# Kernel optimization log

Measured on AMD Instinct MI355X. Metric: run time of the kernel, lower is better.

## Reference

```python
import jax, jax.numpy as jnp
import numpy as np

N_HASHES = 8
BUCKET_SIZE = 64


def setup_inputs() -> dict:
    key = jax.random.key(0)
    k1, k2, k3 = jax.random.split(key, 3)
    B, S, D = 16, 4096, 64
    n_buckets = S // BUCKET_SIZE  # 64
    qk = jax.random.normal(k1, (B, S, D), jnp.float32)
    v = jax.random.normal(k2, (B, S, D), jnp.float32)
    # random rotations (shared across batch, per hash round): (1, D, n_hashes, n_buckets//2)
    rotations = jax.random.normal(k3, (1, D, N_HASHES, n_buckets // 2), jnp.float32)
    return {"qk": qk, "v": v, "rotations": rotations}


def _look_one_back(x):
    # concat each chunk with the previous chunk (wrap-around), along the within-chunk axis
    x_extra = jnp.roll(x, 1, axis=1)
    return jnp.concatenate([x, x_extra], axis=2)


def _lsh_attention(qk, v, rotations):
    B, S, D = qk.shape
    n_buckets = S // BUCKET_SIZE

    # ---- hash_vectors ----
    rot = jnp.broadcast_to(rotations, (B, D, N_HASHES, n_buckets // 2))
    rotated = jnp.einsum('btf,bfhi->bhti', qk, rot)           # [B, H, S, nb/2]
    rotated = jnp.concatenate([rotated, -rotated], axis=-1)    # [B, H, S, nb]
    buckets = jnp.argmax(rotated, axis=-1)                     # [B, H, S]
    offsets = (jnp.arange(N_HASHES) * n_buckets).reshape(1, -1, 1)
    buckets = (buckets + offsets).reshape(B, -1)               # [B, H*S]

    # ---- sort by (bucket, position) ----
    total = N_HASHES * S
    ticker = jnp.arange(total)
    buckets_and_t = S * buckets + (ticker % S)[None, :]        # unique keys
    sticker = jnp.argsort(buckets_and_t, axis=-1)              # sort order
    undo_sort = jnp.argsort(sticker, axis=-1)

    st = sticker % S                                           # original positions
    sqk = jnp.take_along_axis(qk, st[..., None], axis=1)       # [B, H*S, D]
    sv = jnp.take_along_axis(v, st[..., None], axis=1)

    chunk_size = N_HASHES * n_buckets                          # number of chunks
    bq_t = st.reshape(B, chunk_size, -1)                       # [B, C, bs]
    bqk = sqk.reshape(B, chunk_size, -1, D)                    # [B, C, bs, D]
    bv = sv.reshape(B, chunk_size, -1, D)

    bq = bqk
    bk = bqk / jnp.clip(jnp.linalg.norm(bqk, axis=-1, keepdims=True), 1e-12)

    bk = _look_one_back(bk)                                    # [B, C, 2*bs, D]
    bv = _look_one_back(bv)
    bkv_t = _look_one_back(bq_t)                               # [B, C, 2*bs]

    dots = jnp.einsum('bhie,bhje->bhij', bq, bk) * (D ** -0.5)  # [B, C, bs, 2*bs]

    # mask self-attention (token attending to itself)
    self_mask = bq_t[:, :, :, None] == bkv_t[:, :, None, :]
    dots = jnp.where(self_mask, jnp.float32(-1e5), dots)

    lse = jax.nn.logsumexp(dots, axis=-1, keepdims=True)
    probs = jnp.exp(dots - lse)
    bo = jnp.einsum('buij,buje->buie', probs, bv)              # [B, C, bs, D]

    so = bo.reshape(B, -1, D)                                  # [B, H*S, D]
    slogits = lse.reshape(B, -1)                               # [B, H*S]

    # unsort back to original order
    o = jnp.take_along_axis(so, undo_sort[..., None], axis=1)
    logits = jnp.take_along_axis(slogits, undo_sort, axis=1)

    o = o.reshape(B, N_HASHES, S, D)
    logits = logits.reshape(B, N_HASHES, S, 1)

    # combine hash rounds by normalized logsumexp weights
    w = jnp.exp(logits - jax.nn.logsumexp(logits, axis=1, keepdims=True))
    out = jnp.sum(o * w, axis=1)                               # [B, S, D]
    return out, buckets


def reference(qk, v, rotations):
    return _lsh_attention(qk, v, rotations)
```

## Files before the change

kernel.cpp:

```cpp
#include <hip/hip_runtime.h>
#include <hip/hip_bf16.h>
#include <math.h>

#define B 16
#define S 4096
#define D 64
#define NH 8
#define NBUCK 64
#define CHUNKS 512
#define BS 64

#define GAP_MFMA 0.12f

typedef __attribute__((ext_vector_type(8))) short s8_t;
typedef __attribute__((ext_vector_type(4))) float f4_t;
typedef __attribute__((ext_vector_type(2))) unsigned int u32x2;

__device__ inline unsigned short bf16_rne(float x) {
    unsigned int u = __float_as_uint(x);
    u += 0x7fffu + ((u >> 16) & 1u);
    return (unsigned short)(u >> 16);
}
__device__ inline unsigned int pack_bf16_pair(float x0, float x1) {
    return (unsigned int)bf16_rne(x0) | ((unsigned int)bf16_rne(x1) << 16);
}
__device__ inline void split_bf16(float x, unsigned short& h, unsigned short& l) {
    h = bf16_rne(x);
    float hf = __uint_as_float(((unsigned int)h) << 16);
    l = bf16_rne(x - hf);
}
__device__ inline unsigned int pack_trunc(float x0, float x1) {
    return __builtin_amdgcn_perm(__float_as_uint(x1), __float_as_uint(x0),
                                 0x07060302u);
}
__device__ inline unsigned short bf16_trunc(float x) {
    return (unsigned short)(__float_as_uint(x) >> 16);
}

#define BAR_LGKM() do {                                          \
    asm volatile("s_waitcnt lgkmcnt(0)" ::: "memory");           \
    __builtin_amdgcn_s_barrier();                                \
    asm volatile("" ::: "memory");                               \
} while (0)

template<int OFF>
__device__ inline u32x2 tr_read(unsigned int vaddr) {
    u32x2 d;
    asm volatile("ds_read_b64_tr_b16 %0, %1 offset:%c2"
                 : "=v"(d) : "v"(vaddr), "i"(OFF));
    return d;
}

#define HA_OFF 0
#define HQH_OFF 36864
#define HQL_OFF 55296
#define HLDS_TOT 73728
#define HSTR 144

__global__ __launch_bounds__(256, 2) void hash_kernel(
    const float* __restrict__ qk, const float* __restrict__ rot,
    float* __restrict__ out_buckets, int* __restrict__ bucket_ws,
    unsigned char* __restrict__ flag_ws)
{
    __shared__ char lds[HLDS_TOT];
    int tid = threadIdx.x;
    int wg = blockIdx.x;
    int orig = ((wg & 7) << 6) + (wg >> 3);
    int b    = orig >> 5;
    int tile = orig & 31;
    int token0 = tile * 128;

    {
        char* arow = lds + HA_OFF + tid * HSTR;
        #pragma unroll 4
        for (int f = 0; f < 64; f += 2) {
            float r0 = rot[(size_t)f * 256 + tid];
            float r1 = rot[(size_t)(f + 1) * 256 + tid];
            *(unsigned int*)(arow + f * 2) = pack_bf16_pair(r0, r1);
        }
    }
    {
        int wv0   = tid >> 6;
        int lane0 = tid & 63;
        int s_ = lane0 & 3;
        int rowA = wv0 * 32 + (lane0 >> 2);
        int rowB = rowA + 16;
        const float4* qA = (const float4*)(qk + ((size_t)b * S + token0 + rowA) * D);
        const float4* qB = (const float4*)(qk + ((size_t)b * S + token0 + rowB) * D);
        float4 a4[4], b4[4];
        #pragma unroll
        for (int n = 0; n < 4; ++n) { a4[n] = qA[n * 4 + s_]; b4[n] = qB[n * 4 + s_]; }

        char* qhA = lds + HQH_OFF + rowA * HSTR;
        char* qlA = lds + HQL_OFF + rowA * HSTR;
        char* qhB = lds + HQH_OFF + rowB * HSTR;
        char* qlB = lds + HQL_OFF + rowB * HSTR;
        #pragma unroll
        for (int n = 0; n < 4; ++n) {
            float fa[4] = {a4[n].x, a4[n].y, a4[n].z, a4[n].w};
            float fb[4] = {b4[n].x, b4[n].y, b4[n].z, b4[n].w};
            unsigned short h[4], l[4];
            #pragma unroll
            for (int e = 0; e < 4; ++e) split_bf16(fa[e], h[e], l[e]);
            *(uint2*)(qhA + n * 32 + s_ * 8) =
                make_uint2((unsigned)h[0] | ((unsigned)h[1] << 16),
                           (unsigned)h[2] | ((unsigned)h[3] << 16));
            *(uint2*)(qlA + n * 32 + s_ * 8) =
                make_uint2((unsigned)l[0] | ((unsigned)l[1] << 16),
                           (unsigned)l[2] | ((unsigned)l[3] << 16));
            #pragma unroll
            for (int e = 0; e < 4; ++e) split_bf16(fb[e], h[e], l[e]);
            *(uint2*)(qhB + n * 32 + s_ * 8) =
                make_uint2((unsigned)h[0] | ((unsigned)h[1] << 16),
                           (unsigned)h[2] | ((unsigned)h[3] << 16));
            *(uint2*)(qlB + n * 32 + s_ * 8) =
                make_uint2((unsigned)l[0] | ((unsigned)l[1] << 16),
                           (unsigned)l[2] | ((unsigned)l[3] << 16));
        }
    }
    __syncthreads();

    int wv   = tid >> 6;
    int lane = tid & 63;
    int quad = lane >> 4;
    int cc   = lane & 15;

    for (int nt = 0; nt < 2; ++nt) {
        int ntg = wv * 2 + nt;
        const char* qrh = lds + HQH_OFF + (ntg * 16 + cc) * HSTR + quad * 16;
        const char* qrl = lds + HQL_OFF + (ntg * 16 + cc) * HSTR + quad * 16;
        s8_t bh0 = *(const s8_t*)(qrh);
        s8_t bh1 = *(const s8_t*)(qrh + 64);
        s8_t bl0 = *(const s8_t*)(qrl);
        s8_t bl1 = *(const s8_t*)(qrl + 64);

        float v1 = -3e38f, v2 = -3e38f;
        int i1 = 0;

        for (int mt = 0; mt < 16; ++mt) {
            const char* arow = lds + HA_OFF + (mt * 16 + cc) * HSTR + quad * 16;
            s8_t a0 = *(const s8_t*)(arow);
            s8_t a1 = *(const s8_t*)(arow + 64);
            f4_t acc = (f4_t){0.f, 0.f, 0.f, 0.f};
            acc = __builtin_amdgcn_mfma_f32_16x16x32_bf16(a0, bh0, acc, 0, 0, 0);
            acc = __builtin_amdgcn_mfma_f32_16x16x32_bf16(a1, bh1, acc, 0, 0, 0);
            acc = __builtin_amdgcn_mfma_f32_16x16x32_bf16(a0, bl0, acc, 0, 0, 0);
            acc = __builtin_amdgcn_mfma_f32_16x16x32_bf16(a1, bl1, acc, 0, 0, 0);

            if ((mt & 1) == 0) { v1 = -3e38f; v2 = -3e38f; i1 = 0; }
            int ibase = ((mt & 1) << 4) + (quad << 2);
            #pragma unroll
            for (int r = 0; r < 4; ++r) {
                float vp = acc[r];
                int ip = ibase + r;
                v2 = fmaxf(v2, fminf(vp, v1));
                if (vp > v1) { v1 = vp; i1 = ip; }
                float vn = -vp;
                v2 = fmaxf(v2, fminf(vn, v1));
                if (vn > v1) { v1 = vn; i1 = ip + 32; }
            }

            if (mt & 1) {
                #pragma unroll
                for (int off = 16; off <= 32; off <<= 1) {
                    float ov1 = __shfl_xor(v1, off, 64);
                    float ov2 = __shfl_xor(v2, off, 64);
                    int   oi1 = __shfl_xor(i1, off, 64);
                    float nv2 = fmaxf(fmaxf(v2, ov2), fminf(v1, ov1));
                    if (ov1 > v1) { v1 = ov1; i1 = oi1; }
                    v2 = nv2;
                }
                if (quad == 0) {
                    int h = mt >> 1;
                    int tok = token0 + ntg * 16 + cc;
                    size_t idx = (size_t)(b * NH + h) * S + tok;
                    bucket_ws[idx] = i1;
                    out_buckets[idx] = (float)(i1 + h * NBUCK);
                    flag_ws[idx] = (v1 - v2 < GAP_MFMA) ? 1 : 0;
                }
            }
        }
    }
}

__global__ __launch_bounds__(256) void hash_fixup_kernel(
    const float* __restrict__ qk, const float* __restrict__ rot,
    const unsigned char* __restrict__ flag_ws,
    float* __restrict__ out_buckets, int* __restrict__ bucket_ws)
{
    __shared__ int list[2048];
    __shared__ int cnt;
    int tid = threadIdx.x;
    if (tid == 0) cnt = 0;
    __syncthreads();

    int base = blockIdx.x * 2048;
    for (int i = tid; i < 2048; i += 256) {
        if (flag_ws[base + i]) {
            int slot = atomicAdd(&cnt, 1);
            list[slot] = base + i;
        }
    }
    __syncthreads();
    int n = cnt;

    for (int j = tid; j < n; j += 256) {
        int gid = list[j];
        int bh = gid >> 12, t = gid & (S - 1);
        int b = bh >> 3, h = bh & 7;
        const float* row = qk + ((size_t)b * S + t) * D;

        double acc[32];
        #pragma unroll
        for (int i = 0; i < 32; ++i) acc[i] = 0.0;
        for (int f = 0; f < 64; ++f) {
            double x = (double)row[f];
            const float* rr = rot + f * (NH * 32) + h * 32;
            #pragma unroll
            for (int i = 0; i < 32; ++i)
                acc[i] = __fma_rn(x, (double)rr[i], acc[i]);
        }
        double best = acc[0]; int bi = 0;
        double worst = acc[0]; int wi = 0;
        #pragma unroll
        for (int i = 1; i < 32; ++i) {
            if (acc[i] > best)  { best = acc[i]; bi = i; }
            if (acc[i] < worst) { worst = acc[i]; wi = i; }
        }
        int bucket = (-worst > best) ? (32 + wi) : bi;
        bucket_ws[gid] = bucket;
        out_buckets[gid] = (float)(bucket + h * NBUCK);
    }
}

__global__ __launch_bounds__(512) void sort_kernel(
    const int* __restrict__ bucket_ws, int* __restrict__ st_ws)
{
    __shared__ int sb[S];
    __shared__ int hist[8][64];
    __shared__ int bpref[64];
    __shared__ int woff[8][64];

    int tid  = threadIdx.x;
    int wv   = tid >> 6;
    int lane = tid & 63;
    int base = blockIdx.x * S;

    hist[wv][lane] = 0;
    __syncthreads();

    int qbase = wv * 512;
    #pragma unroll
    for (int i = 0; i < 8; ++i) {
        int t = qbase + i * 64 + lane;
        int v = bucket_ws[base + t];
        sb[t] = v;
        atomicAdd(&hist[wv][v], 1);
    }
    __syncthreads();

    if (wv == 0) {
        int total = 0;
        #pragma unroll
        for (int w = 0; w < 8; ++w) total += hist[w][lane];
        int x = total;
        #pragma unroll
        for (int off = 1; off < 64; off <<= 1) {
            int y = __shfl_up(x, off, 64);
            if (lane >= off) x += y;
        }
        bpref[lane] = x - total;
    }
    __syncthreads();
    {
        int o = bpref[lane];
        for (int w2 = 0; w2 < 8; ++w2) {
            if (w2 < wv) o += hist[w2][lane];
        }
        woff[wv][lane] = o;
    }
    __syncthreads();

    for (int g = 0; g < 8; ++g) {
        int t = qbase + g * 64 + lane;
        int v = sb[t];

        unsigned long long m = ~0ULL;
        #pragma unroll
        for (int bit = 0; bit < 6; ++bit) {
            unsigned long long bm = __ballot((v >> bit) & 1);
            m &= ((v >> bit) & 1) ? bm : ~bm;
        }
        unsigned long long below = (lane == 63) ? ~0ULL >> 1
                                 : ((1ULL << lane) - 1ULL);
        int rank = __popcll(m & below);
        int cnt  = __popcll(m);

        int pos = woff[wv][v] + rank;
        st_ws[base + pos] = t;

        if ((m & below) == 0ULL)
            woff[wv][v] += cnt;
    }
}

#define OFF_VT 18432
#define OFF_NRM 35840
#define OFF_TKX 36352
#define OFF_PINV 36864
#define LDS_TOT 37120
#define KSTRB 144
#define PSTRB 272

template<int KC>
__device__ inline void pv_step(const char* lds, unsigned vaddr,
                               int wv, int cc, int quad, f4_t* oaccT)
{
    s8_t pb = *(const s8_t*)(lds + (wv * 16 + cc) * PSTRB + KC * 64 + quad * 16);
    u32x2 t00 = tr_read<KC * 4352 +    0>(vaddr);
    u32x2 t01 = tr_read<KC * 4352 +  544>(vaddr);
    u32x2 t10 = tr_read<KC * 4352 + 1088>(vaddr);
    u32x2 t11 = tr_read<KC * 4352 + 1632>(vaddr);
    u32x2 t20 = tr_read<KC * 4352 + 2176>(vaddr);
    u32x2 t21 = tr_read<KC * 4352 + 2720>(vaddr);
    u32x2 t30 = tr_read<KC * 4352 + 3264>(vaddr);
    u32x2 t31 = tr_read<KC * 4352 + 3808>(vaddr);
    asm volatile("s_waitcnt lgkmcnt(0)" ::: "memory");
    __builtin_amdgcn_sched_barrier(0);
    union { u32x2 d[2]; s8_t s; } u0, u1, u2, u3;
    u0.d[0] = t00; u0.d[1] = t01;
    u1.d[0] = t10; u1.d[1] = t11;
    u2.d[0] = t20; u2.d[1] = t21;
    u3.d[0] = t30; u3.d[1] = t31;
    oaccT[0] = __builtin_amdgcn_mfma_f32_16x16x32_bf16(u0.s, pb, oaccT[0], 0, 0, 0);
    oaccT[1] = __builtin_amdgcn_mfma_f32_16x16x32_bf16(u1.s, pb, oaccT[1], 0, 0, 0);
    oaccT[2] = __builtin_amdgcn_mfma_f32_16x16x32_bf16(u2.s, pb, oaccT[2], 0, 0, 0);
    oaccT[3] = __builtin_amdgcn_mfma_f32_16x16x32_bf16(u3.s, pb, oaccT[3], 0, 0, 0);
}

__global__ __launch_bounds__(256, 4) void attn_kernel(
    const float* __restrict__ qk, const float* __restrict__ v,
    const int* __restrict__ st_ws,
    __hip_bfloat16* __restrict__ o_ws, float* __restrict__ logits_ws)
{
    __shared__ char lds[LDS_TOT];
    float* nrm_s  = (float*)(lds + OFF_NRM);
    int*   tkx    = (int*)(lds + OFF_TKX);
    float* pinv_s = (float*)(lds + OFF_PINV);

    int tid = threadIdx.x;
    int wg = blockIdx.x;
    int orig = ((wg & 7) << 10) + (wg >> 3);
    int c = orig & (CHUNKS - 1);
    int b = orig >> 9;
    int h = c >> 6;
    int sbase = b * (NH * S);
    int cprev = (c + CHUNKS - 1) & (CHUNKS - 1);

    int wv   = tid >> 6;
    int lane = tid & 63;
    int quad = lane >> 4;
    int cc   = lane & 15;
    int s_   = lane & 3;

    int rowA = wv * 32 + (lane >> 2);
    int rowB = rowA + 16;
    int chK  = (wv < 2) ? c : cprev;
    int tokKA = st_ws[sbase + chK * BS + (rowA & 63)];
    int tokKB = st_ws[sbase + chK * BS + (rowB & 63)];
    const float4* kpA = (const float4*)(qk + ((size_t)b * S + tokKA) * D);
    const float4* kpB = (const float4*)(qk + ((size_t)b * S + tokKB) * D);
    float4 kA4[4], kB4[4];
    #pragma unroll
    for (int n = 0; n < 4; ++n) { kA4[n] = kpA[n * 4 + s_]; kB4[n] = kpB[n * 4 + s_]; }

    int prA = wv * 32 + (lane >> 2);
    int prB = prA + 16;
    int ciA = ((prA & 3) << 4) | (prA >> 3);
    int ciB = ((prB & 3) << 4) | (prB >> 3);
    int chVA = (prA & 4) ? cprev : c;
    int chVB = (prB & 4) ? cprev : c;
    int tokVA = st_ws[sbase + chVA * BS + ciA];
    int tokVB = st_ws[sbase + chVB * BS + ciB];
    const float4* vpA = (const float4*)(v + ((size_t)b * S + tokVA) * D);
    const float4* vpB = (const float4*)(v + ((size_t)b * S + tokVB) * D);
    float4 vA4[4], vB4[4];
    #pragma unroll
    for (int n = 0; n < 4; ++n) { vA4[n] = vpA[n * 4 + s_]; vB4[n] = vpB[n * 4 + s_]; }

    {
        float ssA = 0.f, ssB = 0.f;
        #pragma unroll
        for (int n = 0; n < 4; ++n) {
            ssA += kA4[n].x*kA4[n].x + kA4[n].y*kA4[n].y
                 + kA4[n].z*kA4[n].z + kA4[n].w*kA4[n].w;
            ssB += kB4[n].x*kB4[n].x + kB4[n].y*kB4[n].y
                 + kB4[n].z*kB4[n].z + kB4[n].w*kB4[n].w;
        }
        ssA += __shfl_xor(ssA, 1, 64); ssA += __shfl_xor(ssA, 2, 64);
        ssB += __shfl_xor(ssB, 1, 64); ssB += __shfl_xor(ssB, 2, 64);
        if (s_ == 0) {
            nrm_s[rowA] = __builtin_amdgcn_rsqf(fmaxf(ssA, 1e-24f)) * 0.18033688f;
            nrm_s[rowB] = __builtin_amdgcn_rsqf(fmaxf(ssB, 1e-24f)) * 0.18033688f;
            tkx[rowA] = tokKA;
            tkx[rowB] = tokKB;
        }
        #pragma unroll
        for (int n = 0; n < 4; ++n) {
            *(uint2*)(lds + rowA * KSTRB + n * 32 + s_ * 8) =
                make_uint2(pack_trunc(kA4[n].x, kA4[n].y),
                           pack_trunc(kA4[n].z, kA4[n].w));
            *(uint2*)(lds + rowB * KSTRB + n * 32 + s_ * 8) =
                make_uint2(pack_trunc(kB4[n].x, kB4[n].y),
                           pack_trunc(kB4[n].z, kB4[n].w));
        }
    }
    BAR_LGKM();

    int qrow = wv * 16 + cc;
    f4_t acc[8];
    #pragma unroll
    for (int t = 0; t < 8; ++t) acc[t] = (f4_t){0.f,0.f,0.f,0.f};

    __builtin_amdgcn_s_setprio(1);
    #pragma unroll
    for (int kc = 0; kc < 2; ++kc) {
        int aoff = kc * 64 + quad * 16;
        s8_t av = *(const s8_t*)(lds + qrow * KSTRB + aoff);
        #pragma unroll
        for (int t = 0; t < 8; ++t) {
            s8_t bv = *(const s8_t*)(lds + (t * 16 + cc) * KSTRB + aoff);
            acc[t] = __builtin_amdgcn_mfma_f32_16x16x32_bf16(av, bv, acc[t], 0, 0, 0);
        }
    }
    __builtin_amdgcn_s_setprio(0);

    {
        int kcA = prA >> 5, qA = (prA >> 3) & 3, rA = (prA >> 2) & 1, jA = prA & 3;
        int kcB = prB >> 5, qB = (prB >> 3) & 3, rB = (prB >> 2) & 1, jB = prB & 3;
        #pragma unroll
        for (int n = 0; n < 4; ++n) {
            *(uint2*)(lds + OFF_VT + (kcA * 8 + n * 2 + rA) * 544
                      + qA * 128 + jA * 32 + s_ * 8) =
                make_uint2(pack_trunc(vA4[n].x, vA4[n].y),
                           pack_trunc(vA4[n].z, vA4[n].w));
            *(uint2*)(lds + OFF_VT + (kcB * 8 + n * 2 + rB) * 544
                      + qB * 128 + jB * 32 + s_ * 8) =
                make_uint2(pack_trunc(vB4[n].x, vB4[n].y),
                           pack_trunc(vB4[n].z, vB4[n].w));
        }
    }

    float invsc[8];
    #pragma unroll
    for (int t = 0; t < 8; ++t)
        invsc[t] = nrm_s[t * 16 + cc];

    float sm[4] = {0.f, 0.f, 0.f, 0.f};
    #pragma unroll
    for (int t = 0; t < 8; ++t) {
        #pragma unroll
        for (int g = 0; g < 4; ++g)
            acc[t][g] = __builtin_amdgcn_exp2f(acc[t][g] * invsc[t]);
        if (t == wv) {
            #pragma unroll
            for (int g = 0; g < 4; ++g)
                if (cc == quad * 4 + g) acc[t][g] = 0.f;
        }
        #pragma unroll
        for (int g = 0; g < 4; ++g) sm[g] += acc[t][g];
    }
    #pragma unroll
    for (int msk = 1; msk <= 8; msk <<= 1)
        #pragma unroll
        for (int g = 0; g < 4; ++g) sm[g] += __shfl_xor(sm[g], msk, 64);

    if (cc == 0) {
        #pragma unroll
        for (int g = 0; g < 4; ++g) {
            int q = wv * 16 + quad * 4 + g;
            int tq = tkx[q];
            pinv_s[q] = __builtin_amdgcn_rcpf(sm[g]);
            logits_ws[sbase + h * S + tq] = 0.69314718f * __log2f(sm[g]);
        }
    }

    BAR_LGKM();
    #pragma unroll
    for (int g = 0; g < 4; ++g) {
        int q = wv * 16 + quad * 4 + g;
        uint4 w;
        w.x = pack_trunc(acc[0][g], acc[1][g]);
        w.y = pack_trunc(acc[2][g], acc[3][g]);
        w.z = pack_trunc(acc[4][g], acc[5][g]);
        w.w = pack_trunc(acc[6][g], acc[7][g]);
        *(uint4*)(lds + q * PSTRB + cc * 16) = w;
    }

    f4_t oaccT[4];
    #pragma unroll
    for (int n = 0; n < 4; ++n) oaccT[n] = (f4_t){0.f,0.f,0.f,0.f};

    unsigned vaddr = (unsigned)(unsigned long long)(lds + OFF_VT)
                   + (unsigned)lane * 8u;

    __builtin_amdgcn_s_setprio(1);
    pv_step<0>(lds, vaddr, wv, cc, quad, oaccT);
    pv_step<1>(lds, vaddr, wv, cc, quad, oaccT);
    pv_step<2>(lds, vaddr, wv, cc, quad, oaccT);
    pv_step<3>(lds, vaddr, wv, cc, quad, oaccT);
    __builtin_amdgcn_s_setprio(0);

    {
        int q = wv * 16 + cc;
        int tok = tkx[q];
        float pq = pinv_s[q];
        __hip_bfloat16* op = o_ws + ((size_t)(sbase + h * S + tok)) * D + quad * 4;
        #pragma unroll
        for (int n = 0; n < 4; ++n) {
            uint2 pk2;
            pk2.x = pack_trunc(oaccT[n][0] * pq, oaccT[n][1] * pq);
            pk2.y = pack_trunc(oaccT[n][2] * pq, oaccT[n][3] * pq);
            *(uint2*)(op + n * 16) = pk2;
        }
    }
}

__global__ __launch_bounds__(256) void combine_kernel(
    const __hip_bfloat16* __restrict__ o_ws, const float* __restrict__ logits_ws,
    float* __restrict__ out)
{
    int gid = blockIdx.x * 256 + threadIdx.x;
    int token = gid >> 3;
    int d8 = gid & 7;
    int b = token >> 12;
    int t = token & (S - 1);
    int base = b * (NH * S) + t;

    float l[8];
    #pragma unroll
    for (int hh = 0; hh < 8; ++hh) l[hh] = logits_ws[base + hh * S];
    float m = l[0];
    #pragma unroll
    for (int hh = 1; hh < 8; ++hh) m = fmaxf(m, l[hh]);
    float w[8]; float ssum = 0.f;
    #pragma unroll
    for (int hh = 0; hh < 8; ++hh) { w[hh] = __expf(l[hh] - m); ssum += w[hh]; }
    float inv = __builtin_amdgcn_rcpf(ssum);

    float accv[8] = {0,0,0,0,0,0,0,0};
    #pragma unroll
    for (int hh = 0; hh < 8; ++hh) {
        uint4 pk = *(const uint4*)(o_ws + (size_t)(base + hh * S) * D + d8 * 8);
        float wh = w[hh] * inv;
        unsigned int ws_[4] = {pk.x, pk.y, pk.z, pk.w};
        #pragma unroll
        for (int e = 0; e < 4; ++e) {
            float lo = __uint_as_float(ws_[e] << 16);
            float hi = __uint_as_float(ws_[e] & 0xffff0000u);
            accv[2*e]   += wh * lo;
            accv[2*e+1] += wh * hi;
        }
    }
    float4* op = (float4*)(out + (size_t)token * D + d8 * 8);
    op[0] = make_float4(accv[0], accv[1], accv[2], accv[3]);
    op[1] = make_float4(accv[4], accv[5], accv[6], accv[7]);
}

extern "C" void kernel_launch(void* const* d_in, const int* in_sizes, int n_in,
                              void* d_out, int out_size, void* d_ws, size_t ws_size,
                              hipStream_t stream) {
    const float* qk  = (const float*)d_in[0];
    const float* v   = (const float*)d_in[1];
    const float* rot = (const float*)d_in[2];

    float* out         = (float*)d_out;
    float* out_buckets = out + (size_t)B * S * D;

    int*   bucket_ws = (int*)d_ws;
    int*   st_ws     = bucket_ws + (size_t)B * NH * S;
    float* logits_ws = (float*)(st_ws + (size_t)B * NH * S);
    __hip_bfloat16* o_ws = (__hip_bfloat16*)(logits_ws + (size_t)B * NH * S);
    unsigned char* flag_ws = (unsigned char*)(o_ws + (size_t)B * NH * S * D);

    hash_kernel<<<B * 32, 256, 0, stream>>>(qk, rot, out_buckets, bucket_ws,
                                            flag_ws);
    hash_fixup_kernel<<<(B * NH * S) / 2048, 256, 0, stream>>>(
        qk, rot, flag_ws, out_buckets, bucket_ws);
    sort_kernel<<<B * NH, 512, 0, stream>>>(bucket_ws, st_ws);
    attn_kernel<<<B * CHUNKS, 256, 0, stream>>>(qk, v, st_ws, o_ws, logits_ws);
    combine_kernel<<<(B * S * 8) / 256, 256, 0, stream>>>(o_ws, logits_ws, out);
}
```

Baseline: 187.9 us.

## Use single fp16 MFMA for hash projection and widen sort blocks to 1024 threads

The hash projection drops the bf16 hi/lo split of qk (four bf16 MFMAs per tile) in favour of one fp16 conversion and two fp16 MFMAs, which halves the LDS footprint and MFMA work. The near-tie margin that sends tokens to the fp64 fixup path is lowered to match the higher fp16 precision. The sort kernel also moves from 512 to 1024 threads per block, so each wave handles fewer elements. The risk is that fp16 range or rounding misclassifies argmax ties beyond the smaller margin, and more tokens might land in the fixup path.

```diff
diff --git a/kernel.cpp b/kernel.cpp
--- a/kernel.cpp
+++ b/kernel.cpp
@@ -10,24 +10,20 @@
 #define CHUNKS 512
 #define BS 64
 
-#define GAP_MFMA 0.12f
+#define GAP_MFMA 0.03f
 
 typedef __attribute__((ext_vector_type(8))) short s8_t;
+typedef __attribute__((ext_vector_type(8))) _Float16 h8_t;
 typedef __attribute__((ext_vector_type(4))) float f4_t;
 typedef __attribute__((ext_vector_type(2))) unsigned int u32x2;
 
-__device__ inline unsigned short bf16_rne(float x) {
-    unsigned int u = __float_as_uint(x);
-    u += 0x7fffu + ((u >> 16) & 1u);
-    return (unsigned short)(u >> 16);
-}
-__device__ inline unsigned int pack_bf16_pair(float x0, float x1) {
-    return (unsigned int)bf16_rne(x0) | ((unsigned int)bf16_rne(x1) << 16);
-}
-__device__ inline void split_bf16(float x, unsigned short& h, unsigned short& l) {
-    h = bf16_rne(x);
-    float hf = __uint_as_float(((unsigned int)h) << 16);
-    l = bf16_rne(x - hf);
+__device__ inline unsigned short f16_rne(float x) {
+    union { _Float16 f; unsigned short u; } cv;
+    cv.f = (_Float16)x;
+    return cv.u;
+}
+__device__ inline unsigned int pack_f16_pair(float x0, float x1) {
+    return (unsigned int)f16_rne(x0) | ((unsigned int)f16_rne(x1) << 16);
 }
 __device__ inline unsigned int pack_trunc(float x0, float x1) {
     return __builtin_amdgcn_perm(__float_as_uint(x1), __float_as_uint(x0),
@@ -52,9 +48,8 @@
 }
 
 #define HA_OFF 0
-#define HQH_OFF 36864
-#define HQL_OFF 55296
-#define HLDS_TOT 73728
+#define HQ_OFF 36864
+#define HLDS_TOT 55296
 #define HSTR 144
 
 __global__ __launch_bounds__(256, 2) void hash_kernel(
@@ -76,7 +71,7 @@
         for (int f = 0; f < 64; f += 2) {
             float r0 = rot[(size_t)f * 256 + tid];
             float r1 = rot[(size_t)(f + 1) * 256 + tid];
-            *(unsigned int*)(arow + f * 2) = pack_bf16_pair(r0, r1);
+            *(unsigned int*)(arow + f * 2) = pack_f16_pair(r0, r1);
         }
     }
     {
@@ -91,31 +86,16 @@
         #pragma unroll
         for (int n = 0; n < 4; ++n) { a4[n] = qA[n * 4 + s_]; b4[n] = qB[n * 4 + s_]; }
 
-        char* qhA = lds + HQH_OFF + rowA * HSTR;
-        char* qlA = lds + HQL_OFF + rowA * HSTR;
-        char* qhB = lds + HQH_OFF + rowB * HSTR;
-        char* qlB = lds + HQL_OFF + rowB * HSTR;
+        char* qhA = lds + HQ_OFF + rowA * HSTR;
+        char* qhB = lds + HQ_OFF + rowB * HSTR;
         #pragma unroll
         for (int n = 0; n < 4; ++n) {
-            float fa[4] = {a4[n].x, a4[n].y, a4[n].z, a4[n].w};
-            float fb[4] = {b4[n].x, b4[n].y, b4[n].z, b4[n].w};
-            unsigned short h[4], l[4];
-            #pragma unroll
-            for (int e = 0; e < 4; ++e) split_bf16(fa[e], h[e], l[e]);
             *(uint2*)(qhA + n * 32 + s_ * 8) =
-                make_uint2((unsigned)h[0] | ((unsigned)h[1] << 16),
-                           (unsigned)h[2] | ((unsigned)h[3] << 16));
-            *(uint2*)(qlA + n * 32 + s_ * 8) =
-                make_uint2((unsigned)l[0] | ((unsigned)l[1] << 16),
-                           (unsigned)l[2] | ((unsigned)l[3] << 16));
-            #pragma unroll
-            for (int e = 0; e < 4; ++e) split_bf16(fb[e], h[e], l[e]);
+                make_uint2(pack_f16_pair(a4[n].x, a4[n].y),
+                           pack_f16_pair(a4[n].z, a4[n].w));
             *(uint2*)(qhB + n * 32 + s_ * 8) =
-                make_uint2((unsigned)h[0] | ((unsigned)h[1] << 16),
-                           (unsigned)h[2] | ((unsigned)h[3] << 16));
-            *(uint2*)(qlB + n * 32 + s_ * 8) =
-                make_uint2((unsigned)l[0] | ((unsigned)l[1] << 16),
-                           (unsigned)l[2] | ((unsigned)l[3] << 16));
+                make_uint2(pack_f16_pair(b4[n].x, b4[n].y),
+                           pack_f16_pair(b4[n].z, b4[n].w));
         }
     }
     __syncthreads();
@@ -127,25 +107,20 @@
 
     for (int nt = 0; nt < 2; ++nt) {
         int ntg = wv * 2 + nt;
-        const char* qrh = lds + HQH_OFF + (ntg * 16 + cc) * HSTR + quad * 16;
-        const char* qrl = lds + HQL_OFF + (ntg * 16 + cc) * HSTR + quad * 16;
-        s8_t bh0 = *(const s8_t*)(qrh);
-        s8_t bh1 = *(const s8_t*)(qrh + 64);
-        s8_t bl0 = *(const s8_t*)(qrl);
-        s8_t bl1 = *(const s8_t*)(qrl + 64);
+        const char* qr = lds + HQ_OFF + (ntg * 16 + cc) * HSTR + quad * 16;
+        h8_t b0 = *(const h8_t*)(qr);
+        h8_t b1 = *(const h8_t*)(qr + 64);
 
         float v1 = -3e38f, v2 = -3e38f;
         int i1 = 0;
 
         for (int mt = 0; mt < 16; ++mt) {
             const char* arow = lds + HA_OFF + (mt * 16 + cc) * HSTR + quad * 16;
-            s8_t a0 = *(const s8_t*)(arow);
-            s8_t a1 = *(const s8_t*)(arow + 64);
+            h8_t a0 = *(const h8_t*)(arow);
+            h8_t a1 = *(const h8_t*)(arow + 64);
             f4_t acc = (f4_t){0.f, 0.f, 0.f, 0.f};
-            acc = __builtin_amdgcn_mfma_f32_16x16x32_bf16(a0, bh0, acc, 0, 0, 0);
-            acc = __builtin_amdgcn_mfma_f32_16x16x32_bf16(a1, bh1, acc, 0, 0, 0);
-            acc = __builtin_amdgcn_mfma_f32_16x16x32_bf16(a0, bl0, acc, 0, 0, 0);
-            acc = __builtin_amdgcn_mfma_f32_16x16x32_bf16(a1, bl1, acc, 0, 0, 0);
+            acc = __builtin_amdgcn_mfma_f32_16x16x32_f16(a0, b0, acc, 0, 0, 0);
+            acc = __builtin_amdgcn_mfma_f32_16x16x32_f16(a1, b1, acc, 0, 0, 0);
 
             if ((mt & 1) == 0) { v1 = -3e38f; v2 = -3e38f; i1 = 0; }
             int ibase = ((mt & 1) << 4) + (quad << 2);
@@ -233,13 +208,13 @@
     }
 }
 
-__global__ __launch_bounds__(512) void sort_kernel(
+__global__ __launch_bounds__(1024) void sort_kernel(
     const int* __restrict__ bucket_ws, int* __restrict__ st_ws)
 {
     __shared__ int sb[S];
-    __shared__ int hist[8][64];
+    __shared__ int hist[16][64];
     __shared__ int bpref[64];
-    __shared__ int woff[8][64];
+    __shared__ int woff[16][64];
 
     int tid  = threadIdx.x;
     int wv   = tid >> 6;
@@ -249,9 +224,9 @@
     hist[wv][lane] = 0;
     __syncthreads();
 
-    int qbase = wv * 512;
-    #pragma unroll
-    for (int i = 0; i < 8; ++i) {
+    int qbase = wv * 256;
+    #pragma unroll
+    for (int i = 0; i < 4; ++i) {
         int t = qbase + i * 64 + lane;
         int v = bucket_ws[base + t];
         sb[t] = v;
@@ -262,7 +237,7 @@
     if (wv == 0) {
         int total = 0;
         #pragma unroll
-        for (int w = 0; w < 8; ++w) total += hist[w][lane];
+        for (int w = 0; w < 16; ++w) total += hist[w][lane];
         int x = total;
         #pragma unroll
         for (int off = 1; off < 64; off <<= 1) {
@@ -274,14 +249,15 @@
     __syncthreads();
     {
         int o = bpref[lane];
-        for (int w2 = 0; w2 < 8; ++w2) {
+        #pragma unroll
+        for (int w2 = 0; w2 < 16; ++w2) {
             if (w2 < wv) o += hist[w2][lane];
         }
         woff[wv][lane] = o;
     }
     __syncthreads();
 
-    for (int g = 0; g < 8; ++g) {
+    for (int g = 0; g < 4; ++g) {
         int t = qbase + g * 64 + lane;
         int v = sb[t];
 
@@ -587,7 +563,7 @@
                                             flag_ws);
     hash_fixup_kernel<<<(B * NH * S) / 2048, 256, 0, stream>>>(
         qk, rot, flag_ws, out_buckets, bucket_ws);
-    sort_kernel<<<B * NH, 512, 0, stream>>>(bucket_ws, st_ws);
+    sort_kernel<<<B * NH, 1024, 0, stream>>>(bucket_ws, st_ws);
     attn_kernel<<<B * CHUNKS, 256, 0, stream>>>(qk, v, st_ws, o_ws, logits_ws);
     combine_kernel<<<(B * S * 8) / 256, 256, 0, stream>>>(o_ws, logits_ws, out);
 }
```

New measurement: 185.2 us. Within noise of the previous version (-1.4%).
